# Optimization experiments

Hardware: AMD Instinct MI355X
Metric: run time of the kernel (lower is better)

Reference implementation:

```python
import jax, jax.numpy as jnp
import numpy as np

B, KOBJ, NS, NK = 32, 100, 16, 8
EMB, FEAT, HID, OUT, COMB = 1024, 2052, 1024, 3000, 512


def _pseudo_coord(bb_centre):
    # bb_centre (B,K,2) -> polar pseudo coords (B,K,K,2) = (rho, theta)
    d = bb_centre[:, :, None, :] - bb_centre[:, None, :, :]
    rho = jnp.sqrt(d[..., 0] ** 2 + d[..., 1] ** 2)
    theta = jnp.arctan2(d[..., 0], d[..., 1])
    return jnp.stack([rho, theta], axis=-1)


def _gauss_weights(pseudo, mr, mt, pr, pt):
    # pseudo (B,K,NS,2); kernel params (NK,) -> weights (B,K,NS,NK)
    rho = pseudo[..., 0:1]
    theta = pseudo[..., 1:2]
    w_rho = jnp.exp(-0.5 * (rho - mr) ** 2 / (1e-14 + pr ** 2))
    fa = jnp.abs(theta - mt)
    sa = jnp.abs(2.0 * jnp.pi - fa)
    w_th = jnp.exp(-0.5 * jnp.minimum(fa, sa) ** 2 / (1e-14 + pt ** 2))
    w = w_rho * w_th
    w = jnp.where(jnp.isnan(w), 0.0, w)
    return w / jnp.sum(w, axis=-1, keepdims=True)  # normalise over kernels


def _graph_conv(feats, pseudo, conv_w, mr, mt, pr, pt):
    # feats (B,K,NS,F), conv_w (NK,F,out_k) -> (B,K,NK*out_k)
    w = _gauss_weights(pseudo, mr, mt, pr, pt)          # (B,K,NS,NK)
    agg = jnp.einsum('bksm,bksf->bkmf', w, feats)       # per-kernel neighbour sum
    out = jnp.einsum('bkmf,mfo->bkmo', agg, conv_w)     # per-kernel linear
    return out.reshape(out.shape[0], out.shape[1], -1)  # kernel-major concat


def _neighbourhood(feats, pseudo, adj, weight):
    # topk over adjacency rows; softmax over topk values (== the per-row loop softmax)
    top_v, top_i = jax.lax.top_k(adj, NS)               # (B,K,NS)
    a = jax.nn.softmax(top_v, axis=-1)
    nb_f = jax.vmap(lambda f, i: f[i])(feats, top_i)    # (B,K,NS,F)
    nb_p = jnp.take_along_axis(pseudo, top_i[..., None], axis=2)  # (B,K,NS,2)
    if weight:
        nb_f = a[..., None] * nb_f
    return nb_f, nb_p


def _forward(question, image, K, W_lproj, b_lproj, W_e1, b_e1, W_e2, b_e2,
             conv_w1, mean_rho1, mean_theta1, prec_rho1, prec_theta1,
             conv_w2, mean_rho2, mean_theta2, prec_rho2, prec_theta2,
             W_o1, b_o1, W_o2, b_o2):
    bb = image[:, :, -4:]
    bb_size = bb[:, :, 2:] - bb[:, :, :2]
    bb_centre = bb[:, :, :2] + 0.5 * bb_size
    pseudo = _pseudo_coord(bb_centre)                   # (B,K,K,2)

    qenc = question @ W_lproj + b_lproj                 # (B,HID)
    qrep = jnp.broadcast_to(qenc[:, None, :], (image.shape[0], K, qenc.shape[-1]))
    cat = jnp.concatenate([image, qrep], axis=-1)       # (B,K,FEAT+HID)

    # GraphLearner: two relu linears then gram matrix
    h = jax.nn.relu(cat @ W_e1 + b_e1)
    h = jax.nn.relu(h @ W_e2 + b_e2)                    # (B,K,COMB)
    adj = jnp.einsum('bkc,blc->bkl', h, h)              # (B,K,K)

    nb_f, nb_p = _neighbourhood(image, pseudo, adj, weight=True)
    g1 = jax.nn.relu(_graph_conv(nb_f, nb_p, conv_w1, mean_rho1, mean_theta1, prec_rho1, prec_theta1))
    nb_f2, nb_p2 = _neighbourhood(g1, pseudo, adj, weight=False)
    g2 = jax.nn.relu(_graph_conv(nb_f2, nb_p2, conv_w2, mean_rho2, mean_theta2, prec_rho2, prec_theta2))
    g2 = jnp.max(g2, axis=1)                            # (B,HID)

    hh = jax.nn.relu(qenc) * g2
    h1 = jax.nn.relu(hh @ W_o1 + b_o1)
    logits = h1 @ W_o2 + b_o2
    return logits, adj


def setup_inputs() -> dict:
    key = jax.random.key(0)
    ks = jax.random.split(key, 17)
    s = jnp.float32(0.02)
    f32 = jnp.float32
    inp = {
        'question': jax.random.normal(ks[0], (B, EMB), f32),
        'image': jax.random.uniform(ks[1], (B, KOBJ, FEAT), f32),
        'K': KOBJ,
        'W_lproj': jax.random.normal(ks[2], (EMB, HID), f32) * s,
        'b_lproj': jnp.zeros((HID,), f32),
        'W_e1': jax.random.normal(ks[3], (FEAT + HID, COMB), f32) * s,
        'b_e1': jnp.zeros((COMB,), f32),
        'W_e2': jax.random.normal(ks[4], (COMB, COMB), f32) * s,
        'b_e2': jnp.zeros((COMB,), f32),
        'conv_w1': jax.random.normal(ks[5], (NK, FEAT, 2 * HID // NK), f32) * s,
        'mean_rho1': jax.random.uniform(ks[6], (NK,), f32),
        'mean_theta1': jax.random.uniform(ks[7], (NK,), f32, -np.pi, np.pi),
        'prec_rho1': jax.random.uniform(ks[8], (NK,), f32),
        'prec_theta1': jax.random.uniform(ks[9], (NK,), f32),
        'conv_w2': jax.random.normal(ks[10], (NK, 2 * HID, HID // NK), f32) * s,
        'mean_rho2': jax.random.uniform(ks[11], (NK,), f32),
        'mean_theta2': jax.random.uniform(ks[12], (NK,), f32, -np.pi, np.pi),
        'prec_rho2': jax.random.uniform(ks[13], (NK,), f32),
        'prec_theta2': jax.random.uniform(ks[14], (NK,), f32),
        'W_o1': jax.random.normal(ks[15], (HID, OUT), f32) * s,
        'b_o1': jnp.zeros((OUT,), f32),
        'W_o2': jax.random.normal(ks[16], (OUT, OUT), f32) * s,
        'b_o2': jnp.zeros((OUT,), f32),
    }
    return inp


def reference(question, image, K, W_lproj, b_lproj, W_e1, b_e1, W_e2, b_e2,
              conv_w1, mean_rho1, mean_theta1, prec_rho1, prec_theta1,
              conv_w2, mean_rho2, mean_theta2, prec_rho2, prec_theta2,
              W_o1, b_o1, W_o2, b_o2):
    return _forward(question, image, K, W_lproj, b_lproj, W_e1, b_e1, W_e2, b_e2,
                    conv_w1, mean_rho1, mean_theta1, prec_rho1, prec_theta1,
                    conv_w2, mean_rho2, mean_theta2, prec_rho2, prec_theta2,
                    W_o1, b_o1, W_o2, b_o2)
```

## Files before the change

kernel.cpp:

```cpp
#include <hip/hip_runtime.h>
#include <math.h>
#include <stdint.h>

#define B_    32
#define KOBJ  100
#define NS_   16
#define NK_   8
#define EMB_  1024
#define FEAT_ 2052
#define HID_  1024
#define OUT_  3000
#define COMB_ 512

#define KP1   2112
#define KP2   2048
#define NO_P  3072
#define KO2   3008

typedef __attribute__((ext_vector_type(8))) short s16x8;
typedef __attribute__((ext_vector_type(4))) float f32x4;

__device__ inline short f2bf(float f) {
  uint32_t u = __builtin_bit_cast(uint32_t, f);
  u = (u + 0x7fff + ((u >> 16) & 1)) >> 16;
  return (short)u;
}
__device__ inline float bf2f(short s) {
  uint32_t u = ((uint32_t)(uint16_t)s) << 16;
  return __builtin_bit_cast(float, u);
}
__device__ inline void gload_lds16(const void* g, void* l) {
  __builtin_amdgcn_global_load_lds(
      (const __attribute__((address_space(1))) void*)g,
      (__attribute__((address_space(3))) void*)l, 16, 0, 0);
}
__device__ inline int xcd_remap(int fid, int nwg) {
  int q = nwg >> 3, r = nwg & 7;
  int x = fid & 7, l = fid >> 3;
  return (x < r ? x * (q + 1) : r * (q + 1) + (x - r) * q) + l;
}

#define IMG_CHUNKS (B_ * KOBJ * (KP1 / 8))
#define IMG_BLKS   ((IMG_CHUNKS + 255) / 256)
#define Q_CHUNKS   (B_ * (EMB_ / 8))
#define Q_BLKS     ((Q_CHUNKS + 255) / 256)
#define C_BLKS     ((B_ * KOBJ + 255) / 256)

__device__ inline void cvt8_split(const float* __restrict__ in, short* __restrict__ oh,
                                  short* __restrict__ ol, int K, int Kp, int idx) {
  int row = idx / (Kp / 8), c8 = (idx % (Kp / 8)) * 8;
  float f[8];
  if (c8 + 8 <= K) {
    const float* src = in + (size_t)row * K + c8;
    float4 a = *(const float4*)src;
    float4 b = *(const float4*)(src + 4);
    f[0] = a.x; f[1] = a.y; f[2] = a.z; f[3] = a.w;
    f[4] = b.x; f[5] = b.y; f[6] = b.z; f[7] = b.w;
  } else {
#pragma unroll
    for (int i = 0; i < 8; ++i) {
      int k = c8 + i;
      f[i] = (k < K) ? in[(size_t)row * K + k] : 0.f;
    }
  }
  s16x8 vh, vl;
#pragma unroll
  for (int i = 0; i < 8; ++i) {
    short h = f2bf(f[i]);
    vh[i] = h;
    vl[i] = f2bf(f[i] - bf2f(h));
  }
  *(s16x8*)(oh + (size_t)row * Kp + c8) = vh;
  *(s16x8*)(ol + (size_t)row * Kp + c8) = vl;
}

__global__ __launch_bounds__(256) void prep_inputs(
    const float* __restrict__ image, const float* __restrict__ question,
    short* __restrict__ imgb, short* __restrict__ imgl,
    short* __restrict__ qh, short* __restrict__ ql, float* __restrict__ cent) {
  int bb = blockIdx.x, tid = threadIdx.x;
  if (bb < IMG_BLKS) {
    int idx = bb * 256 + tid;
    if (idx < IMG_CHUNKS) cvt8_split(image, imgb, imgl, FEAT_, KP1, idx);
  } else if (bb < IMG_BLKS + Q_BLKS) {
    int idx = (bb - IMG_BLKS) * 256 + tid;
    if (idx < Q_CHUNKS) cvt8_split(question, qh, ql, EMB_, EMB_, idx);
  } else {
    int i = (bb - IMG_BLKS - Q_BLKS) * 256 + tid;
    if (i < B_ * KOBJ) {
      const float* bbx = image + (size_t)i * FEAT_ + (FEAT_ - 4);
      cent[i * 2 + 0] = 0.5f * (bbx[0] + bbx[2]);
      cent[i * 2 + 1] = 0.5f * (bbx[1] + bbx[3]);
    }
  }
}

__global__ void cvt_pad_rows_split(const float* __restrict__ in, short* __restrict__ outh,
                                   short* __restrict__ outl, int K, int Kp, int total) {
  int idx = blockIdx.x * 256 + threadIdx.x;
  if (idx < total) cvt8_split(in, outh, outl, K, Kp, idx);
}

struct TD {
  const float* in; short* oh; short* ol;
  int K, N, Kp, OPM, nkt, split, conv, cum;
};
struct TDs { TD d[8]; };

__global__ __launch_bounds__(256) void transpose_all(TDs ds) {
  __shared__ float s[64][65];
  int bid = blockIdx.x;
  int i = 0;
  while (i < 7 && bid >= ds.d[i].cum) ++i;
  const TD& d = ds.d[i];
  int local = bid - (i ? ds.d[i - 1].cum : 0);
  int k0 = (local % d.nkt) * 64, n0 = (local / d.nkt) * 64;
  int t = threadIdx.x;
  int rr = t >> 4, c4 = (t & 15) * 4;
  bool fullN = d.conv || (n0 + 64 <= d.N);
#pragma unroll
  for (int p = 0; p < 4; ++p) {
    int row = p * 16 + rr;
    int kg = k0 + row;
    float v0 = 0.f, v1 = 0.f, v2 = 0.f, v3 = 0.f;
    if (kg < d.K) {
      const float* src = d.conv
          ? d.in + ((size_t)(n0 / d.OPM) * d.K + kg) * d.OPM + (n0 % d.OPM) + c4
          : d.in + (size_t)kg * d.N + n0 + c4;
      if (fullN) {
        float4 v = *(const float4*)src;
        v0 = v.x; v1 = v.y; v2 = v.z; v3 = v.w;
      } else {
        int nb = n0 + c4;
        if (nb + 0 < d.N) v0 = src[0];
        if (nb + 1 < d.N) v1 = src[1];
        if (nb + 2 < d.N) v2 = src[2];
        if (nb + 3 < d.N) v3 = src[3];
      }
    }
    s[row][c4 + 0] = v0; s[row][c4 + 1] = v1;
    s[row][c4 + 2] = v2; s[row][c4 + 3] = v3;
  }
  __syncthreads();
  int nl = t >> 2, kc = (t & 3) << 4;
#pragma unroll
  for (int half = 0; half < 2; ++half) {
    s16x8 vh, vl;
#pragma unroll
    for (int j = 0; j < 8; ++j) {
      float f = s[kc + half * 8 + j][nl];
      short h = f2bf(f);
      vh[j] = h;
      vl[j] = f2bf(f - bf2f(h));
    }
    size_t o = (size_t)(n0 + nl) * d.Kp + k0 + kc + half * 8;
    *(s16x8*)(d.oh + o) = vh;
    if (d.split) *(s16x8*)(d.ol + o) = vl;
  }
}

template <int BM, int BN, int WR, int WC, bool SPLIT, bool RELU, bool BIAS, int OMODE, bool SPLITK>
__global__ __launch_bounds__(WR * WC * 64) void gemm_mx(
    const short* __restrict__ Ah, const short* __restrict__ Al,
    const short* __restrict__ Bh, const short* __restrict__ Bl,
    const float* __restrict__ bias,
    float* __restrict__ Cf, short* __restrict__ Ch, short* __restrict__ Cl,
    float* __restrict__ part, int KS,
    int M, int N, int Kp, int ldc, int Nw) {
  constexpr int NWV = WR * WC;
  constexpr int WM = BM / WR, WN = BN / WC;
  constexpr int FM = WM / 16, FN = WN / 16;
  constexpr int ACH = BM / 8, BCH = BN / 8;
  constexpr int NCH = (ACH + BCH) * (SPLIT ? 2 : 1);
  __shared__ short Ash[BM * 64];
  __shared__ short Bsh[BN * 64];
  __shared__ short Asl[SPLIT ? BM * 64 : 64];
  __shared__ short Bsl[SPLIT ? BN * 64 : 64];
  int tid = threadIdx.x, wave = tid >> 6, lane = tid & 63;
  int wr = wave / WC, wc = wave % WC;
  int r16 = lane & 15, kq = lane >> 4;
  int gx = gridDim.x, gy = gridDim.y, gz = gridDim.z;
  int fid = (blockIdx.z * gy + blockIdx.y) * gx + blockIdx.x;
  int wg = xcd_remap(fid, gx * gy * gz);
  int bx = wg % gx, byz = wg / gx;
  int by = byz % gy, bz = byz / gy;
  int m0 = by * BM, n0 = bx * BN;
  int kb = SPLITK ? bz * KS : 0;
  int ke = SPLITK ? (kb + KS < Kp ? kb + KS : Kp) : Kp;
  f32x4 acc[FM][FN] = {};

  for (int k0 = kb; k0 < ke; k0 += 64) {
    __syncthreads();
    for (int c = wave; c < NCH; c += NWV) {
      int cc = c;
      const short* g;
      char* l;
      bool isA;
      if (cc < ACH) { isA = true; g = Ah; l = (char*)Ash; }
      else if (SPLIT && cc < 2 * ACH) { cc -= ACH; isA = true; g = Al; l = (char*)Asl; }
      else {
        cc -= SPLIT ? 2 * ACH : ACH;
        if (cc < BCH) { isA = false; g = Bh; l = (char*)Bsh; }
        else { cc -= BCH; isA = false; g = Bl; l = (char*)Bsl; }
      }
      int Lb = cc * 1024 + lane * 16;
      int row = Lb >> 7;
      int off = (Lb & 127) ^ ((row & 7) << 4);
      const short* gsrc = g + (size_t)((isA ? m0 : n0) + row) * Kp + k0 + (off >> 1);
      gload_lds16(gsrc, l + cc * 1024);
    }
    __syncthreads();
#pragma unroll
    for (int kk = 0; kk < 2; ++kk) {
      int woff = kk * 64 + kq * 16;
      s16x8 ah[FM], al[FM], bh[FN], bl[FN];
#pragma unroll
      for (int f = 0; f < FM; ++f) {
        int row = wr * WM + f * 16 + r16;
        int o = woff ^ ((row & 7) << 4);
        ah[f] = *(const s16x8*)((const char*)Ash + row * 128 + o);
        if (SPLIT) al[f] = *(const s16x8*)((const char*)Asl + row * 128 + o);
      }
#pragma unroll
      for (int gg = 0; gg < FN; ++gg) {
        int row = wc * WN + gg * 16 + r16;
        int o = woff ^ ((row & 7) << 4);
        bh[gg] = *(const s16x8*)((const char*)Bsh + row * 128 + o);
        if (SPLIT) bl[gg] = *(const s16x8*)((const char*)Bsl + row * 128 + o);
      }
#pragma unroll
      for (int f = 0; f < FM; ++f)
#pragma unroll
        for (int gg = 0; gg < FN; ++gg) {
          acc[f][gg] = __builtin_amdgcn_mfma_f32_16x16x32_bf16(ah[f], bh[gg], acc[f][gg], 0, 0, 0);
          if (SPLIT) {
            acc[f][gg] = __builtin_amdgcn_mfma_f32_16x16x32_bf16(ah[f], bl[gg], acc[f][gg], 0, 0, 0);
            acc[f][gg] = __builtin_amdgcn_mfma_f32_16x16x32_bf16(al[f], bh[gg], acc[f][gg], 0, 0, 0);
          }
        }
    }
  }
#pragma unroll
  for (int f = 0; f < FM; ++f)
#pragma unroll
    for (int gg = 0; gg < FN; ++gg)
#pragma unroll
      for (int r = 0; r < 4; ++r) {
        int m = m0 + wr * WM + f * 16 + (lane >> 4) * 4 + r;
        int n = n0 + wc * WN + gg * 16 + r16;
        if (m >= M || n >= Nw) continue;
        float v = (n < N) ? acc[f][gg][r] : 0.f;
        size_t idx = (size_t)m * ldc + n;
        if (SPLITK) {
          part[(size_t)bz * M * ldc + idx] = v;
        } else {
          if (BIAS && n < N) v += bias[n];
          if (RELU) v = fmaxf(v, 0.f);
          if (OMODE == 0) Cf[idx] = v;
          else if (OMODE == 1) {
            short h = f2bf(v);
            Ch[idx] = h;
            Cl[idx] = f2bf(v - bf2f(h));
          } else {
            Ch[idx] = f2bf(v);
          }
        }
      }
}

template <int OMODE, bool RELU, bool BIAS, bool BCAST>
__global__ void reduce_split(const float* __restrict__ part, int SK, size_t pstride,
                             const float* __restrict__ bias, const float* __restrict__ bcast,
                             int bcols, float* __restrict__ Cf, short* __restrict__ Ch,
                             short* __restrict__ Cl, int M, int N, int ldIn, int ldOut) {
  int idx4 = blockIdx.x * 256 + threadIdx.x;
  int ld4 = ldIn >> 2;
  if (idx4 >= M * ld4) return;
  int m = idx4 / ld4;
  int n = (idx4 - m * ld4) << 2;
  size_t base = (size_t)m * ldIn + n;
  float a[4] = {0.f, 0.f, 0.f, 0.f};
  for (int s = 0; s < SK; ++s) {
    float4 p = *(const float4*)(part + (size_t)s * pstride + base);
    a[0] += p.x; a[1] += p.y; a[2] += p.z; a[3] += p.w;
  }
#pragma unroll
  for (int j = 0; j < 4; ++j) {
    int nn = n + j;
    if (nn < N) {
      if (BCAST) a[j] += bcast[(size_t)(m / KOBJ) * bcols + nn];
      if (BIAS) a[j] += bias[nn];
    }
    if (RELU) a[j] = fmaxf(a[j], 0.f);
  }
  if (n >= ldOut) return;
  size_t o = (size_t)m * ldOut + n;
  if (OMODE == 0) {
    *(float4*)(Cf + o) = make_float4(a[0], a[1], a[2], a[3]);
  } else if (OMODE == 1) {
    short4 hh, ll;
    short* hp = (short*)&hh; short* lp = (short*)&ll;
#pragma unroll
    for (int j = 0; j < 4; ++j) {
      short h = f2bf(a[j]);
      hp[j] = h;
      lp[j] = f2bf(a[j] - bf2f(h));
    }
    *(short4*)(Ch + o) = hh;
    *(short4*)(Cl + o) = ll;
  } else {
    short4 hh;
    short* hp = (short*)&hh;
#pragma unroll
    for (int j = 0; j < 4; ++j) hp[j] = f2bf(a[j]);
    *(short4*)(Ch + o) = hh;
  }
}

__global__ __launch_bounds__(512) void adj_mfma(const short* __restrict__ Hh,
                                                const short* __restrict__ Hl,
                                                float* __restrict__ adj) {
  __shared__ short Ash[128 * 64];
  __shared__ short Asl[128 * 64];
  int tid = threadIdx.x, wave = tid >> 6, lane = tid & 63;
  int wr = wave >> 2, wc = wave & 3;
  int r16 = lane & 15, kq = lane >> 4;
  int b = blockIdx.x;
  const short* baseh = Hh + (size_t)b * KOBJ * COMB_;
  const short* basel = Hl + (size_t)b * KOBJ * COMB_;
  f32x4 acc[4][2] = {};
  for (int k0 = 0; k0 < COMB_; k0 += 64) {
    __syncthreads();
    for (int c = wave; c < 32; c += 8) {
      int cc = c & 15;
      bool hi = c < 16;
      int Lb = cc * 1024 + lane * 16;
      int row = Lb >> 7;
      int off = (Lb & 127) ^ ((row & 7) << 4);
      const short* gsrc = (hi ? baseh : basel) + (size_t)row * COMB_ + k0 + (off >> 1);
      gload_lds16(gsrc, (char*)(hi ? Ash : Asl) + cc * 1024);
    }
    __syncthreads();
#pragma unroll
    for (int kk = 0; kk < 2; ++kk) {
      int woff = kk * 64 + kq * 16;
      s16x8 ah[4], al[4], bh[2], bl[2];
#pragma unroll
      for (int f = 0; f < 4; ++f) {
        int row = wr * 64 + f * 16 + r16;
        int o = woff ^ ((row & 7) << 4);
        ah[f] = *(const s16x8*)((const char*)Ash + row * 128 + o);
        al[f] = *(const s16x8*)((const char*)Asl + row * 128 + o);
      }
#pragma unroll
      for (int g = 0; g < 2; ++g) {
        int row = wc * 32 + g * 16 + r16;
        int o = woff ^ ((row & 7) << 4);
        bh[g] = *(const s16x8*)((const char*)Ash + row * 128 + o);
        bl[g] = *(const s16x8*)((const char*)Asl + row * 128 + o);
      }
#pragma unroll
      for (int f = 0; f < 4; ++f)
#pragma unroll
        for (int g = 0; g < 2; ++g) {
          acc[f][g] = __builtin_amdgcn_mfma_f32_16x16x32_bf16(ah[f], bh[g], acc[f][g], 0, 0, 0);
          acc[f][g] = __builtin_amdgcn_mfma_f32_16x16x32_bf16(ah[f], bl[g], acc[f][g], 0, 0, 0);
          acc[f][g] = __builtin_amdgcn_mfma_f32_16x16x32_bf16(al[f], bh[g], acc[f][g], 0, 0, 0);
        }
    }
  }
#pragma unroll
  for (int f = 0; f < 4; ++f)
#pragma unroll
    for (int g = 0; g < 2; ++g)
#pragma unroll
      for (int r = 0; r < 4; ++r) {
        int m = wr * 64 + f * 16 + (lane >> 4) * 4 + r;
        int n = wc * 32 + g * 16 + r16;
        if (m < KOBJ && n < KOBJ)
          adj[((size_t)b * KOBJ + m) * KOBJ + n] = acc[f][g][r];
      }
}

__global__ __launch_bounds__(256) void topk_weights_kernel(
    const float* __restrict__ adj, const float* __restrict__ cent,
    const float* __restrict__ mr1, const float* __restrict__ mt1,
    const float* __restrict__ pr1, const float* __restrict__ pt1,
    const float* __restrict__ mr2, const float* __restrict__ mt2,
    const float* __restrict__ pr2, const float* __restrict__ pt2,
    int* __restrict__ topi, float* __restrict__ c1, float* __restrict__ c2) {
  int row = blockIdx.x * 4 + (threadIdx.x >> 6);
  int lane = threadIdx.x & 63;
  int b = row / KOBJ, k = row % KOBJ;
  const float* ar = adj + (size_t)row * KOBJ;
  float v0 = (lane < KOBJ) ? ar[lane] : -INFINITY;
  float v1 = (lane + 64 < KOBJ) ? ar[lane + 64] : -INFINITY;
  int i0 = lane, i1 = lane + 64;
  float tv[NS_];
  int ti[NS_];
#pragma unroll
  for (int s = 0; s < NS_; ++s) {
    bool p0 = (v0 > v1) || (v0 == v1 && i0 < i1);
    float bv = p0 ? v0 : v1;
    int bi = p0 ? i0 : i1;
#pragma unroll
    for (int off = 32; off > 0; off >>= 1) {
      float ov = __shfl_xor(bv, off);
      int oi = __shfl_xor(bi, off);
      if (ov > bv || (ov == bv && oi < bi)) { bv = ov; bi = oi; }
    }
    tv[s] = bv; ti[s] = bi;
    if (bi == i0) v0 = -INFINITY;
    if (bi == i1) v1 = -INFINITY;
  }
  float mx = tv[0], sum = 0.f, av[NS_];
#pragma unroll
  for (int s = 0; s < NS_; ++s) { av[s] = expf(tv[s] - mx); sum += av[s]; }
  if (lane < NS_) {
    int j = ti[lane];
    topi[(size_t)row * NS_ + lane] = j;
    float cx = cent[(b * KOBJ + k) * 2 + 0], cy = cent[(b * KOBJ + k) * 2 + 1];
    float dx = cx - cent[(b * KOBJ + j) * 2 + 0];
    float dy = cy - cent[(b * KOBJ + j) * 2 + 1];
    float rho = sqrtf(dx * dx + dy * dy);
    float th = atan2f(dx, dy);
    float w1[NK_], w2[NK_], s1 = 0.f, s2 = 0.f;
#pragma unroll
    for (int m = 0; m < NK_; ++m) {
      {
        float pr = pr1[m], pt = pt1[m], dr = rho - mr1[m];
        float wr = expf(-0.5f * dr * dr / (1e-14f + pr * pr));
        float fa = fabsf(th - mt1[m]);
        float sa = fabsf(6.283185307179586f - fa);
        float da = fminf(fa, sa);
        float wt = expf(-0.5f * da * da / (1e-14f + pt * pt));
        float w = wr * wt;
        if (w != w) w = 0.f;
        w1[m] = w; s1 += w;
      }
      {
        float pr = pr2[m], pt = pt2[m], dr = rho - mr2[m];
        float wr = expf(-0.5f * dr * dr / (1e-14f + pr * pr));
        float fa = fabsf(th - mt2[m]);
        float sa = fabsf(6.283185307179586f - fa);
        float da = fminf(fa, sa);
        float wt = expf(-0.5f * da * da / (1e-14f + pt * pt));
        float w = wr * wt;
        if (w != w) w = 0.f;
        w2[m] = w; s2 += w;
      }
    }
    float as = av[lane] / sum;
#pragma unroll
    for (int m = 0; m < NK_; ++m) {
      c1[((size_t)row * NS_ + lane) * NK_ + m] = as * (w1[m] / s1);
      c2[((size_t)row * NS_ + lane) * NK_ + m] = w2[m] / s2;
    }
  }
}

template <int VEC, bool BF16OUT>
__global__ __launch_bounds__(256) void combine_kernel(
    const short* __restrict__ proj, const float* __restrict__ coeff,
    const int* __restrict__ topi, float* __restrict__ outf, short* __restrict__ outb,
    int N, int mshift) {
  int row = xcd_remap(blockIdx.x, gridDim.x);
  int b = row / KOBJ;
  __shared__ int ids[NS_];
  __shared__ float cs[NS_ * NK_];
  int tid = threadIdx.x;
  if (tid < NS_) ids[tid] = topi[(size_t)row * NS_ + tid];
  else if (tid >= 32 && tid < 32 + NS_ * NK_) cs[tid - 32] = coeff[(size_t)row * NS_ * NK_ + (tid - 32)];
  __syncthreads();
  int n = tid * VEC;
  if (n >= N) return;
  int m = n >> mshift;
  float acc[VEC];
#pragma unroll
  for (int j = 0; j < VEC; ++j) acc[j] = 0.f;
#pragma unroll
  for (int s = 0; s < NS_; ++s) {
    float cc = cs[s * NK_ + m];
    const short* p = proj + ((size_t)b * KOBJ + ids[s]) * N + n;
    if (VEC == 8) {
      s16x8 v = *(const s16x8*)p;
#pragma unroll
      for (int j = 0; j < 8; ++j) acc[j] = fmaf(cc, bf2f(v[j]), acc[j]);
    } else {
      short4 v = *(const short4*)p;
      const short* vp = (const short*)&v;
#pragma unroll
      for (int j = 0; j < 4; ++j) acc[j] = fmaf(cc, bf2f(vp[j]), acc[j]);
    }
  }
#pragma unroll
  for (int j = 0; j < VEC; ++j) acc[j] = fmaxf(acc[j], 0.f);
  if (BF16OUT) {
    if (VEC == 8) {
      s16x8 o;
#pragma unroll
      for (int j = 0; j < 8; ++j) o[j] = f2bf(acc[j]);
      *(s16x8*)(outb + (size_t)row * N + n) = o;
    } else {
      short4 o;
      short* op = (short*)&o;
#pragma unroll
      for (int j = 0; j < 4; ++j) op[j] = f2bf(acc[j]);
      *(short4*)(outb + (size_t)row * N + n) = o;
    }
  } else {
    if (VEC == 4) {
      *(float4*)(outf + (size_t)row * N + n) = make_float4(acc[0], acc[1], acc[2], acc[3]);
    } else {
#pragma unroll
      for (int j = 0; j < VEC; ++j) outf[(size_t)row * N + n + j] = acc[j];
    }
  }
}

__global__ void reduce_hh_kernel(const float* __restrict__ g2, const float* __restrict__ qenc,
                                 short* __restrict__ hhb) {
  int i = blockIdx.x * blockDim.x + threadIdx.x;
  if (i >= B_ * HID_) return;
  int b = i >> 10, n = i & (HID_ - 1);
  const float* p = g2 + (size_t)b * KOBJ * HID_ + n;
  float mx = -INFINITY;
  for (int k = 0; k < KOBJ; ++k) mx = fmaxf(mx, p[(size_t)k * HID_]);
  hhb[i] = f2bf(fmaxf(qenc[i], 0.f) * mx);
}

extern "C" void kernel_launch(void* const* d_in, const int* in_sizes, int n_in,
                              void* d_out, int out_size, void* d_ws, size_t ws_size,
                              hipStream_t stream) {
  const float* question = (const float*)d_in[0];
  const float* image    = (const float*)d_in[1];
  const float* W_lproj  = (const float*)d_in[3];
  const float* b_lproj  = (const float*)d_in[4];
  const float* W_e1     = (const float*)d_in[5];
  const float* b_e1     = (const float*)d_in[6];
  const float* W_e2     = (const float*)d_in[7];
  const float* b_e2     = (const float*)d_in[8];
  const float* conv_w1  = (const float*)d_in[9];
  const float* mr1 = (const float*)d_in[10];
  const float* mt1 = (const float*)d_in[11];
  const float* pr1 = (const float*)d_in[12];
  const float* pt1 = (const float*)d_in[13];
  const float* conv_w2  = (const float*)d_in[14];
  const float* mr2 = (const float*)d_in[15];
  const float* mt2 = (const float*)d_in[16];
  const float* pr2 = (const float*)d_in[17];
  const float* pt2 = (const float*)d_in[18];
  const float* W_o1 = (const float*)d_in[19];
  const float* b_o1 = (const float*)d_in[20];
  const float* W_o2 = (const float*)d_in[21];
  const float* b_o2 = (const float*)d_in[22];

  float* out = (float*)d_out;
  float* logits = out;
  float* adj = out + B_ * OUT_;

  char* ws = (char*)d_ws;
  size_t off = 0;
  auto alloc = [&](size_t bytes) { char* p = ws + off; off += (bytes + 255) & ~((size_t)255); return p; };
  float* qenc  = (float*)alloc((size_t)B_ * HID_ * 4);
  short* qh    = (short*)alloc((size_t)B_ * EMB_ * 2);
  short* ql    = (short*)alloc((size_t)B_ * EMB_ * 2);
  short* qeh   = (short*)alloc((size_t)B_ * HID_ * 2);
  short* qel   = (short*)alloc((size_t)B_ * HID_ * 2);
  short* wlph  = (short*)alloc((size_t)EMB_ * HID_ * 2);
  short* wlpl  = (short*)alloc((size_t)EMB_ * HID_ * 2);
  short* we1ah = (short*)alloc((size_t)COMB_ * KP1 * 2);
  short* we1al = (short*)alloc((size_t)COMB_ * KP1 * 2);
  short* we1bh = (short*)alloc((size_t)COMB_ * HID_ * 2);
  short* we1bl = (short*)alloc((size_t)COMB_ * HID_ * 2);
  short* we2h  = (short*)alloc((size_t)COMB_ * COMB_ * 2);
  short* we2l  = (short*)alloc((size_t)COMB_ * COMB_ * 2);
  float* q1    = (float*)alloc((size_t)B_ * COMB_ * 4);
  short* h1h   = (short*)alloc((size_t)B_ * KOBJ * COMB_ * 2);
  short* h1l   = (short*)alloc((size_t)B_ * KOBJ * COMB_ * 2);
  short* h2h   = (short*)alloc((size_t)(B_ * KOBJ + 128) * COMB_ * 2);
  short* h2l   = (short*)alloc((size_t)(B_ * KOBJ + 128) * COMB_ * 2);
  float* cent  = (float*)alloc((size_t)B_ * KOBJ * 2 * 4);
  int*   topi  = (int*)alloc((size_t)B_ * KOBJ * NS_ * 4);
  float* c1    = (float*)alloc((size_t)B_ * KOBJ * NS_ * NK_ * 4);
  float* c2    = (float*)alloc((size_t)B_ * KOBJ * NS_ * NK_ * 4);
  short* imgb  = (short*)alloc((size_t)B_ * KOBJ * KP1 * 2);
  short* imgl  = (short*)alloc((size_t)B_ * KOBJ * KP1 * 2);
  short* cw1t  = (short*)alloc((size_t)(2 * HID_) * KP1 * 2);
  short* cw2t  = (short*)alloc((size_t)HID_ * KP2 * 2);
  short* proj1b = (short*)alloc((size_t)B_ * KOBJ * 2 * HID_ * 2);
  short* g1b   = (short*)alloc((size_t)B_ * KOBJ * KP2 * 2);
  short* proj2b = (short*)alloc((size_t)B_ * KOBJ * HID_ * 2);
  float* g2    = (float*)alloc((size_t)B_ * KOBJ * HID_ * 4);
  short* hhb   = (short*)alloc((size_t)B_ * HID_ * 2);
  short* wo1t  = (short*)alloc((size_t)NO_P * HID_ * 2);
  short* wo2t  = (short*)alloc((size_t)NO_P * KO2 * 2);
  short* h1ob  = (short*)alloc((size_t)B_ * KO2 * 2);
  float* partE = (float*)alloc((size_t)2 * B_ * KOBJ * 2 * HID_ * 4);
  (void)ws_size; (void)in_sizes; (void)n_in; (void)out_size;

  dim3 blk(256), blk512(512);

  prep_inputs<<<dim3(IMG_BLKS + Q_BLKS + C_BLKS), blk, 0, stream>>>(
      image, question, imgb, imgl, qh, ql, cent);

  {
    TDs ds;
    int cum = 0;
    auto set = [&](int i, const float* in, short* oh, short* ol, int K, int N, int Kp,
                   int OPM, int nnt, int split, int conv) {
      int nkt = Kp / 64;
      cum += nkt * nnt;
      ds.d[i] = TD{in, oh, ol, K, N, Kp, OPM, nkt, split, conv, cum};
    };
    set(0, W_lproj, wlph, wlpl, EMB_, HID_, EMB_, 0, HID_ / 64, 1, 0);
    set(1, W_e1, we1ah, we1al, FEAT_, COMB_, KP1, 0, COMB_ / 64, 1, 0);
    set(2, W_e1 + (size_t)FEAT_ * COMB_, we1bh, we1bl, HID_, COMB_, HID_, 0, COMB_ / 64, 1, 0);
    set(3, W_e2, we2h, we2l, COMB_, COMB_, COMB_, 0, COMB_ / 64, 1, 0);
    set(4, conv_w1, cw1t, nullptr, FEAT_, 2 * HID_, KP1, 2 * HID_ / NK_, 2 * HID_ / 64, 0, 1);
    set(5, conv_w2, cw2t, nullptr, 2 * HID_, HID_, KP2, HID_ / NK_, HID_ / 64, 0, 1);
    set(6, W_o1, wo1t, nullptr, HID_, OUT_, HID_, 0, NO_P / 64, 0, 0);
    set(7, W_o2, wo2t, nullptr, OUT_, OUT_, KO2, 0, NO_P / 64, 0, 0);
    transpose_all<<<dim3(cum), blk, 0, stream>>>(ds);
  }

  gemm_mx<32, 64, 2, 2, true, false, true, 0, false><<<dim3(HID_ / 64, 1, 1), blk, 0, stream>>>(
      qh, ql, wlph, wlpl, b_lproj, qenc, nullptr, nullptr, nullptr, 0, B_, HID_, EMB_, HID_, HID_);
  {
    int total = B_ * (HID_ / 8);
    cvt_pad_rows_split<<<dim3((total + 255) / 256), blk, 0, stream>>>(qenc, qeh, qel, HID_, HID_, total);
  }
  gemm_mx<32, 64, 2, 2, true, false, false, 0, false><<<dim3(COMB_ / 64, 1, 1), blk, 0, stream>>>(
      qeh, qel, we1bh, we1bl, nullptr, q1, nullptr, nullptr, nullptr, 0, B_, COMB_, HID_, COMB_, COMB_);
  gemm_mx<128, 64, 4, 2, true, false, false, 0, true><<<dim3(COMB_ / 64, B_ * KOBJ / 128, 4), blk512, 0, stream>>>(
      imgb, imgl, we1ah, we1al, nullptr, nullptr, nullptr, nullptr, partE, 576,
      B_ * KOBJ, COMB_, KP1, COMB_, COMB_);
  reduce_split<1, true, true, true><<<dim3(B_ * KOBJ * COMB_ / 4 / 256), blk, 0, stream>>>(
      partE, 4, (size_t)B_ * KOBJ * COMB_, b_e1, q1, COMB_, nullptr, h1h, h1l,
      B_ * KOBJ, COMB_, COMB_, COMB_);
  gemm_mx<128, 64, 4, 2, true, false, false, 0, true><<<dim3(COMB_ / 64, B_ * KOBJ / 128, 4), blk512, 0, stream>>>(
      h1h, h1l, we2h, we2l, nullptr, nullptr, nullptr, nullptr, partE, 128,
      B_ * KOBJ, COMB_, COMB_, COMB_, COMB_);
  reduce_split<1, true, true, false><<<dim3(B_ * KOBJ * COMB_ / 4 / 256), blk, 0, stream>>>(
      partE, 4, (size_t)B_ * KOBJ * COMB_, b_e2, nullptr, 0, nullptr, h2h, h2l,
      B_ * KOBJ, COMB_, COMB_, COMB_);
  adj_mfma<<<dim3(B_), blk512, 0, stream>>>(h2h, h2l, adj);
  topk_weights_kernel<<<dim3(B_ * KOBJ / 4), blk, 0, stream>>>(
      adj, cent, mr1, mt1, pr1, pt1, mr2, mt2, pr2, pt2, topi, c1, c2);
  gemm_mx<128, 128, 2, 4, false, false, false, 0, true><<<dim3(2 * HID_ / 128, B_ * KOBJ / 128, 2), blk512, 0, stream>>>(
      imgb, nullptr, cw1t, nullptr, nullptr, nullptr, nullptr, nullptr, partE, 1056,
      B_ * KOBJ, 2 * HID_, KP1, 2 * HID_, 2 * HID_);
  reduce_split<2, false, false, false><<<dim3(B_ * KOBJ * 2 * HID_ / 4 / 256), blk, 0, stream>>>(
      partE, 2, (size_t)B_ * KOBJ * 2 * HID_, nullptr, nullptr, 0, nullptr, proj1b, nullptr,
      B_ * KOBJ, 2 * HID_, 2 * HID_, 2 * HID_);
  combine_kernel<8, true><<<dim3(B_ * KOBJ), blk, 0, stream>>>(
      proj1b, c1, topi, nullptr, g1b, 2 * HID_, 8);
  gemm_mx<64, 64, 2, 2, false, false, false, 2, false><<<dim3(HID_ / 64, B_ * KOBJ / 64, 1), blk, 0, stream>>>(
      g1b, nullptr, cw2t, nullptr, nullptr, nullptr, proj2b, nullptr, nullptr, 0,
      B_ * KOBJ, HID_, KP2, HID_, HID_);
  combine_kernel<4, false><<<dim3(B_ * KOBJ), blk, 0, stream>>>(
      proj2b, c2, topi, g2, nullptr, HID_, 7);
  reduce_hh_kernel<<<dim3((B_ * HID_ + 255) / 256), blk, 0, stream>>>(g2, qenc, hhb);
  gemm_mx<32, 128, 1, 4, false, false, false, 0, true><<<dim3(NO_P / 128, 1, 16), blk, 0, stream>>>(
      hhb, nullptr, wo1t, nullptr, nullptr, nullptr, nullptr, nullptr, partE, 64,
      B_, OUT_, HID_, KO2, KO2);
  reduce_split<2, true, true, false><<<dim3((B_ * KO2 / 4 + 255) / 256), blk, 0, stream>>>(
      partE, 16, (size_t)B_ * KO2, b_o1, nullptr, 0, nullptr, h1ob, nullptr,
      B_, OUT_, KO2, KO2);
  gemm_mx<32, 128, 1, 4, false, false, false, 0, true><<<dim3(NO_P / 128, 1, 16), blk, 0, stream>>>(
      h1ob, nullptr, wo2t, nullptr, nullptr, nullptr, nullptr, nullptr, partE, 192,
      B_, OUT_, KO2, KO2, KO2);
  reduce_split<0, false, true, false><<<dim3((B_ * KO2 / 4 + 255) / 256), blk, 0, stream>>>(
      partE, 16, (size_t)B_ * KO2, b_o2, nullptr, 0, logits, nullptr, nullptr,
      B_, OUT_, KO2, OUT_);
}
```

Before: 356.6 us.

## Store split-K partials as bf16, split-K the second conv GEMM, fuse qenc conversion

Split-K partial sums for the two graph-conv projection GEMMs are written as bf16 rather than fp32, which halves partial-buffer traffic, and the reduce kernel gains a bf16 read path. The second conv GEMM moves from a 64x64 single-pass tile to a 128x128 tile with 4-way split-K and a separate reduction. The question-projection GEMM now writes fp32 plus the hi/lo bf16 split in its epilogue, so the standalone conversion kernel is dropped. Rounding partials to bf16 before summing adds precision error, and the partial buffer is shrunk and shared across stages.

```diff
diff --git a/kernel.cpp b/kernel.cpp
--- a/kernel.cpp
+++ b/kernel.cpp
@@ -95,12 +95,6 @@
   }
 }
 
-__global__ void cvt_pad_rows_split(const float* __restrict__ in, short* __restrict__ outh,
-                                   short* __restrict__ outl, int K, int Kp, int total) {
-  int idx = blockIdx.x * 256 + threadIdx.x;
-  if (idx < total) cvt8_split(in, outh, outl, K, Kp, idx);
-}
-
 struct TD {
   const float* in; short* oh; short* ol;
   int K, N, Kp, OPM, nkt, split, conv, cum;
@@ -159,13 +153,14 @@
   }
 }
 
-template <int BM, int BN, int WR, int WC, bool SPLIT, bool RELU, bool BIAS, int OMODE, bool SPLITK>
+template <int BM, int BN, int WR, int WC, bool SPLIT, bool RELU, bool BIAS, int OMODE,
+          bool SPLITK, bool PB16>
 __global__ __launch_bounds__(WR * WC * 64) void gemm_mx(
     const short* __restrict__ Ah, const short* __restrict__ Al,
     const short* __restrict__ Bh, const short* __restrict__ Bl,
     const float* __restrict__ bias,
     float* __restrict__ Cf, short* __restrict__ Ch, short* __restrict__ Cl,
-    float* __restrict__ part, int KS,
+    float* __restrict__ part, short* __restrict__ partb, int KS,
     int M, int N, int Kp, int ldc, int Nw) {
   constexpr int NWV = WR * WC;
   constexpr int WM = BM / WR, WN = BN / WC;
@@ -252,7 +247,9 @@
         float v = (n < N) ? acc[f][gg][r] : 0.f;
         size_t idx = (size_t)m * ldc + n;
         if (SPLITK) {
-          part[(size_t)bz * M * ldc + idx] = v;
+          size_t pidx = (size_t)bz * M * ldc + idx;
+          if (PB16) partb[pidx] = f2bf(v);
+          else      part[pidx] = v;
         } else {
           if (BIAS && n < N) v += bias[n];
           if (RELU) v = fmaxf(v, 0.f);
@@ -261,15 +258,21 @@
             short h = f2bf(v);
             Ch[idx] = h;
             Cl[idx] = f2bf(v - bf2f(h));
+          } else if (OMODE == 2) {
+            Ch[idx] = f2bf(v);
           } else {
-            Ch[idx] = f2bf(v);
+            Cf[idx] = v;
+            short h = f2bf(v);
+            Ch[idx] = h;
+            Cl[idx] = f2bf(v - bf2f(h));
           }
         }
       }
 }
 
-template <int OMODE, bool RELU, bool BIAS, bool BCAST>
-__global__ void reduce_split(const float* __restrict__ part, int SK, size_t pstride,
+template <int OMODE, bool RELU, bool BIAS, bool BCAST, bool PB16>
+__global__ void reduce_split(const float* __restrict__ part, const short* __restrict__ partb,
+                             int SK, size_t pstride,
                              const float* __restrict__ bias, const float* __restrict__ bcast,
                              int bcols, float* __restrict__ Cf, short* __restrict__ Ch,
                              short* __restrict__ Cl, int M, int N, int ldIn, int ldOut) {
@@ -281,8 +284,15 @@
   size_t base = (size_t)m * ldIn + n;
   float a[4] = {0.f, 0.f, 0.f, 0.f};
   for (int s = 0; s < SK; ++s) {
-    float4 p = *(const float4*)(part + (size_t)s * pstride + base);
-    a[0] += p.x; a[1] += p.y; a[2] += p.z; a[3] += p.w;
+    if (PB16) {
+      short4 p = *(const short4*)(partb + (size_t)s * pstride + base);
+      const short* pp = (const short*)&p;
+#pragma unroll
+      for (int j = 0; j < 4; ++j) a[j] += bf2f(pp[j]);
+    } else {
+      float4 p = *(const float4*)(part + (size_t)s * pstride + base);
+      a[0] += p.x; a[1] += p.y; a[2] += p.z; a[3] += p.w;
+    }
   }
 #pragma unroll
   for (int j = 0; j < 4; ++j) {
@@ -596,7 +606,8 @@
   short* wo1t  = (short*)alloc((size_t)NO_P * HID_ * 2);
   short* wo2t  = (short*)alloc((size_t)NO_P * KO2 * 2);
   short* h1ob  = (short*)alloc((size_t)B_ * KO2 * 2);
-  float* partE = (float*)alloc((size_t)2 * B_ * KOBJ * 2 * HID_ * 4);
+  float* partE = (float*)alloc((size_t)4 * B_ * KOBJ * COMB_ * 4);
+  short* partS = (short*)partE;
   (void)ws_size; (void)in_sizes; (void)n_in; (void)out_size;
 
   dim3 blk(256), blk512(512);
@@ -624,53 +635,52 @@
     transpose_all<<<dim3(cum), blk, 0, stream>>>(ds);
   }
 
-  gemm_mx<32, 64, 2, 2, true, false, true, 0, false><<<dim3(HID_ / 64, 1, 1), blk, 0, stream>>>(
-      qh, ql, wlph, wlpl, b_lproj, qenc, nullptr, nullptr, nullptr, 0, B_, HID_, EMB_, HID_, HID_);
-  {
-    int total = B_ * (HID_ / 8);
-    cvt_pad_rows_split<<<dim3((total + 255) / 256), blk, 0, stream>>>(qenc, qeh, qel, HID_, HID_, total);
-  }
-  gemm_mx<32, 64, 2, 2, true, false, false, 0, false><<<dim3(COMB_ / 64, 1, 1), blk, 0, stream>>>(
-      qeh, qel, we1bh, we1bl, nullptr, q1, nullptr, nullptr, nullptr, 0, B_, COMB_, HID_, COMB_, COMB_);
-  gemm_mx<128, 64, 4, 2, true, false, false, 0, true><<<dim3(COMB_ / 64, B_ * KOBJ / 128, 4), blk512, 0, stream>>>(
-      imgb, imgl, we1ah, we1al, nullptr, nullptr, nullptr, nullptr, partE, 576,
+  gemm_mx<32, 64, 2, 2, true, false, true, 3, false, false><<<dim3(HID_ / 64, 1, 1), blk, 0, stream>>>(
+      qh, ql, wlph, wlpl, b_lproj, qenc, qeh, qel, nullptr, nullptr, 0, B_, HID_, EMB_, HID_, HID_);
+  gemm_mx<32, 64, 2, 2, true, false, false, 0, false, false><<<dim3(COMB_ / 64, 1, 1), blk, 0, stream>>>(
+      qeh, qel, we1bh, we1bl, nullptr, q1, nullptr, nullptr, nullptr, nullptr, 0, B_, COMB_, HID_, COMB_, COMB_);
+  gemm_mx<128, 64, 4, 2, true, false, false, 0, true, false><<<dim3(COMB_ / 64, B_ * KOBJ / 128, 4), blk512, 0, stream>>>(
+      imgb, imgl, we1ah, we1al, nullptr, nullptr, nullptr, nullptr, partE, nullptr, 576,
       B_ * KOBJ, COMB_, KP1, COMB_, COMB_);
-  reduce_split<1, true, true, true><<<dim3(B_ * KOBJ * COMB_ / 4 / 256), blk, 0, stream>>>(
-      partE, 4, (size_t)B_ * KOBJ * COMB_, b_e1, q1, COMB_, nullptr, h1h, h1l,
+  reduce_split<1, true, true, true, false><<<dim3(B_ * KOBJ * COMB_ / 4 / 256), blk, 0, stream>>>(
+      partE, nullptr, 4, (size_t)B_ * KOBJ * COMB_, b_e1, q1, COMB_, nullptr, h1h, h1l,
       B_ * KOBJ, COMB_, COMB_, COMB_);
-  gemm_mx<128, 64, 4, 2, true, false, false, 0, true><<<dim3(COMB_ / 64, B_ * KOBJ / 128, 4), blk512, 0, stream>>>(
-      h1h, h1l, we2h, we2l, nullptr, nullptr, nullptr, nullptr, partE, 128,
+  gemm_mx<128, 64, 4, 2, true, false, false, 0, true, false><<<dim3(COMB_ / 64, B_ * KOBJ / 128, 4), blk512, 0, stream>>>(
+      h1h, h1l, we2h, we2l, nullptr, nullptr, nullptr, nullptr, partE, nullptr, 128,
       B_ * KOBJ, COMB_, COMB_, COMB_, COMB_);
-  reduce_split<1, true, true, false><<<dim3(B_ * KOBJ * COMB_ / 4 / 256), blk, 0, stream>>>(
-      partE, 4, (size_t)B_ * KOBJ * COMB_, b_e2, nullptr, 0, nullptr, h2h, h2l,
+  reduce_split<1, true, true, false, false><<<dim3(B_ * KOBJ * COMB_ / 4 / 256), blk, 0, stream>>>(
+      partE, nullptr, 4, (size_t)B_ * KOBJ * COMB_, b_e2, nullptr, 0, nullptr, h2h, h2l,
       B_ * KOBJ, COMB_, COMB_, COMB_);
   adj_mfma<<<dim3(B_), blk512, 0, stream>>>(h2h, h2l, adj);
   topk_weights_kernel<<<dim3(B_ * KOBJ / 4), blk, 0, stream>>>(
       adj, cent, mr1, mt1, pr1, pt1, mr2, mt2, pr2, pt2, topi, c1, c2);
-  gemm_mx<128, 128, 2, 4, false, false, false, 0, true><<<dim3(2 * HID_ / 128, B_ * KOBJ / 128, 2), blk512, 0, stream>>>(
-      imgb, nullptr, cw1t, nullptr, nullptr, nullptr, nullptr, nullptr, partE, 1056,
+  gemm_mx<128, 128, 2, 4, false, false, false, 0, true, true><<<dim3(2 * HID_ / 128, B_ * KOBJ / 128, 2), blk512, 0, stream>>>(
+      imgb, nullptr, cw1t, nullptr, nullptr, nullptr, nullptr, nullptr, nullptr, partS, 1056,
       B_ * KOBJ, 2 * HID_, KP1, 2 * HID_, 2 * HID_);
-  reduce_split<2, false, false, false><<<dim3(B_ * KOBJ * 2 * HID_ / 4 / 256), blk, 0, stream>>>(
-      partE, 2, (size_t)B_ * KOBJ * 2 * HID_, nullptr, nullptr, 0, nullptr, proj1b, nullptr,
+  reduce_split<2, false, false, false, true><<<dim3(B_ * KOBJ * 2 * HID_ / 4 / 256), blk, 0, stream>>>(
+      nullptr, partS, 2, (size_t)B_ * KOBJ * 2 * HID_, nullptr, nullptr, 0, nullptr, proj1b, nullptr,
       B_ * KOBJ, 2 * HID_, 2 * HID_, 2 * HID_);
   combine_kernel<8, true><<<dim3(B_ * KOBJ), blk, 0, stream>>>(
       proj1b, c1, topi, nullptr, g1b, 2 * HID_, 8);
-  gemm_mx<64, 64, 2, 2, false, false, false, 2, false><<<dim3(HID_ / 64, B_ * KOBJ / 64, 1), blk, 0, stream>>>(
-      g1b, nullptr, cw2t, nullptr, nullptr, nullptr, proj2b, nullptr, nullptr, 0,
+  gemm_mx<128, 128, 2, 4, false, false, false, 0, true, true><<<dim3(HID_ / 128, B_ * KOBJ / 128, 4), blk512, 0, stream>>>(
+      g1b, nullptr, cw2t, nullptr, nullptr, nullptr, nullptr, nullptr, nullptr, partS, 512,
       B_ * KOBJ, HID_, KP2, HID_, HID_);
+  reduce_split<2, false, false, false, true><<<dim3(B_ * KOBJ * HID_ / 4 / 256), blk, 0, stream>>>(
+      nullptr, partS, 4, (size_t)B_ * KOBJ * HID_, nullptr, nullptr, 0, nullptr, proj2b, nullptr,
+      B_ * KOBJ, HID_, HID_, HID_);
   combine_kernel<4, false><<<dim3(B_ * KOBJ), blk, 0, stream>>>(
       proj2b, c2, topi, g2, nullptr, HID_, 7);
   reduce_hh_kernel<<<dim3((B_ * HID_ + 255) / 256), blk, 0, stream>>>(g2, qenc, hhb);
-  gemm_mx<32, 128, 1, 4, false, false, false, 0, true><<<dim3(NO_P / 128, 1, 16), blk, 0, stream>>>(
-      hhb, nullptr, wo1t, nullptr, nullptr, nullptr, nullptr, nullptr, partE, 64,
+  gemm_mx<32, 128, 1, 4, false, false, false, 0, true, false><<<dim3(NO_P / 128, 1, 16), blk, 0, stream>>>(
+      hhb, nullptr, wo1t, nullptr, nullptr, nullptr, nullptr, nullptr, partE, nullptr, 64,
       B_, OUT_, HID_, KO2, KO2);
-  reduce_split<2, true, true, false><<<dim3((B_ * KO2 / 4 + 255) / 256), blk, 0, stream>>>(
-      partE, 16, (size_t)B_ * KO2, b_o1, nullptr, 0, nullptr, h1ob, nullptr,
+  reduce_split<2, true, true, false, false><<<dim3((B_ * KO2 / 4 + 255) / 256), blk, 0, stream>>>(
+      partE, nullptr, 16, (size_t)B_ * KO2, b_o1, nullptr, 0, nullptr, h1ob, nullptr,
       B_, OUT_, KO2, KO2);
-  gemm_mx<32, 128, 1, 4, false, false, false, 0, true><<<dim3(NO_P / 128, 1, 16), blk, 0, stream>>>(
-      h1ob, nullptr, wo2t, nullptr, nullptr, nullptr, nullptr, nullptr, partE, 192,
+  gemm_mx<32, 128, 1, 4, false, false, false, 0, true, false><<<dim3(NO_P / 128, 1, 16), blk, 0, stream>>>(
+      h1ob, nullptr, wo2t, nullptr, nullptr, nullptr, nullptr, nullptr, partE, nullptr, 192,
       B_, OUT_, KO2, KO2, KO2);
-  reduce_split<0, false, true, false><<<dim3((B_ * KO2 / 4 + 255) / 256), blk, 0, stream>>>(
-      partE, 16, (size_t)B_ * KO2, b_o2, nullptr, 0, logits, nullptr, nullptr,
+  reduce_split<0, false, true, false, false><<<dim3((B_ * KO2 / 4 + 255) / 256), blk, 0, stream>>>(
+      partE, nullptr, 16, (size_t)B_ * KO2, b_o2, nullptr, 0, logits, nullptr, nullptr,
       B_, OUT_, KO2, OUT_);
 }
```

Measured after the change: 345.1 us. -3.2%, faster.
